# Kernel tuning notes

Measured on AMD Instinct MI355X. Metric: run time of the kernel, lower is better.

The kernel has to match this reference:

```python
import jax, jax.numpy as jnp
import numpy as np

DIM = 1024
N_HEADS = 16
HEAD_DIM = DIM // N_HEADS
COND_DIM = 1024
MLP_RATIO = 4
B = 8
L = 1024  # per-sequence length (equal lengths -> T = B*L packed tokens)
T = B * L
EPS = 1e-5


def setup_inputs() -> dict:
    key = jax.random.key(0)
    ks = jax.random.split(key, 16)
    s = 0.02
    # rotary tables: [max_pos, head_dim//2]
    inv_freq = 1.0 / (10000.0 ** (jnp.arange(0, HEAD_DIM, 2, dtype=jnp.float32) / HEAD_DIM))
    t = jnp.arange(L, dtype=jnp.float32)
    freqs = t[:, None] * inv_freq[None, :]  # [L, HEAD_DIM//2]
    return {
        "x": jax.random.normal(ks[0], (T, DIM), jnp.float32),
        "lengths": jnp.full((B,), L, dtype=jnp.int64),
        "offsets": jnp.arange(B, dtype=jnp.int64) * L,
        "cos": jnp.cos(freqs),
        "sin": jnp.sin(freqs),
        "positions": jnp.tile(jnp.arange(L, dtype=jnp.int64), B),
        "c": jax.random.normal(ks[1], (B, COND_DIM), jnp.float32),
        "ln1_w": jnp.ones((DIM,), jnp.float32),
        "Wq": jax.random.normal(ks[2], (DIM, DIM), jnp.float32) * s,
        "Wk": jax.random.normal(ks[3], (DIM, DIM), jnp.float32) * s,
        "Wv": jax.random.normal(ks[4], (DIM, DIM), jnp.float32) * s,
        "Wo": jax.random.normal(ks[5], (DIM, DIM), jnp.float32) * s,
        "ln2_w": jnp.ones((DIM,), jnp.float32),
        "W1": jax.random.normal(ks[6], (DIM, MLP_RATIO * DIM), jnp.float32) * s,
        "b1": jnp.zeros((MLP_RATIO * DIM,), jnp.float32),
        "W2": jax.random.normal(ks[7], (MLP_RATIO * DIM, DIM), jnp.float32) * s,
        "b2": jnp.zeros((DIM,), jnp.float32),
        "ada_w": jax.random.normal(ks[8], (COND_DIM, 6 * DIM), jnp.float32) * s,
        "ada_b": jnp.zeros((6 * DIM,), jnp.float32),
    }


def _layer_norm(x, w):
    # LayerNorm with weight only (no bias), as in the torch module
    mu = jnp.mean(x, axis=-1, keepdims=True)
    var = jnp.mean(jnp.square(x - mu), axis=-1, keepdims=True)
    return (x - mu) * jax.lax.rsqrt(var + EPS) * w


def _rope(q, k, cos, sin, positions):
    # q, k: [T, H, D]; cos/sin: [max_pos, D//2]; half-split RoPE
    c = cos[positions][:, None, :]  # [T, 1, D//2]
    s = sin[positions][:, None, :]
    def rot(x):
        x1, x2 = jnp.split(x, 2, axis=-1)
        return jnp.concatenate([x1 * c - x2 * s, x2 * c + x1 * s], axis=-1)
    return rot(q), rot(k)


def reference(x, lengths, offsets, cos, sin, positions, c,
              ln1_w, Wq, Wk, Wv, Wo, ln2_w, W1, b1, W2, b2, ada_w, ada_b):
    # adaLN modulation: [B, 6*DIM] -> six [B, DIM]
    ada = c @ ada_w + ada_b
    sh_msa, sc_msa, g_msa, sh_mlp, sc_mlp, g_mlp = jnp.split(ada, 6, axis=-1)
    # per-token gather via seq_ids (equal lengths -> repeat each row L times)
    seq_ids = jnp.repeat(jnp.arange(B), L)  # = repeat_interleave(arange(B), lengths)
    sh_msa_t, sc_msa_t, g_msa_t = sh_msa[seq_ids], sc_msa[seq_ids], g_msa[seq_ids]
    sh_mlp_t, sc_mlp_t, g_mlp_t = sh_mlp[seq_ids], sc_mlp[seq_ids], g_mlp[seq_ids]

    x_skip = x
    h = _layer_norm(x, ln1_w) * (1.0 + sc_msa_t) + sh_msa_t
    q = (h @ Wq).reshape(T, N_HEADS, HEAD_DIM)
    k = (h @ Wk).reshape(T, N_HEADS, HEAD_DIM)
    v = (h @ Wv).reshape(T, N_HEADS, HEAD_DIM)
    q, k = _rope(q, k, cos, sin, positions)

    # intra-sequence-only attention: with equal lengths the block-diagonal
    # score_mod mask is exactly per-sequence attention -> reshape to [B, L, H, D]
    qb = q.reshape(B, L, N_HEADS, HEAD_DIM)
    kb = k.reshape(B, L, N_HEADS, HEAD_DIM)
    vb = v.reshape(B, L, N_HEADS, HEAD_DIM)
    scores = jnp.einsum('blhd,bmhd->bhlm', qb, kb) / jnp.sqrt(jnp.float32(HEAD_DIM))
    probs = jax.nn.softmax(scores, axis=-1)
    attn = jnp.einsum('bhlm,bmhd->blhd', probs, vb).reshape(T, DIM)

    x = x_skip + g_msa_t * (attn @ Wo)  # dropout p is identity in eval mode

    h2 = _layer_norm(x, ln2_w) * (1.0 + sc_mlp_t) + sh_mlp_t
    mlp = jax.nn.gelu(h2 @ W1 + b1, approximate=True) @ W2 + b2
    return x + g_mlp_t * mlp
```

## Files before the change

kernel.cpp:

```cpp
#include <hip/hip_runtime.h>

typedef unsigned short u16;
typedef __attribute__((ext_vector_type(8))) short short8;
typedef __attribute__((ext_vector_type(4))) float f32x4;
typedef __attribute__((ext_vector_type(4))) unsigned uint4v;

__device__ __forceinline__ float bf2f(u16 u){
  unsigned v = ((unsigned)u) << 16;
  return __builtin_bit_cast(float, v);
}
__device__ __forceinline__ u16 f2bf(float f){
  unsigned u = __builtin_bit_cast(unsigned, f);
  u += 0x7fff + ((u >> 16) & 1);
  return (u16)(u >> 16);
}
__device__ __forceinline__ unsigned packbf(float lo, float hi){
  return ((unsigned)f2bf(hi) << 16) | (unsigned)f2bf(lo);
}
__device__ __forceinline__ void async16(const void* g, void* l){
  __builtin_amdgcn_global_load_lds((const __attribute__((address_space(1))) void*)g,
                                   (__attribute__((address_space(3))) void*)l, 16, 0, 0);
}
#define VMW(n) asm volatile("s_waitcnt vmcnt(" #n ")" ::: "memory")

__global__ __launch_bounds__(256) void ada_partial(
    const float* __restrict__ c, const float* __restrict__ aw,
    float* __restrict__ part){
  int n  = blockIdx.x*256 + threadIdx.x;
  int b  = blockIdx.y;
  int kc = blockIdx.z;
  const float* cr  = c + b*1024 + kc*128;
  const float* awp = aw + (size_t)(kc*128)*6144 + n;
  float acc = 0.f;
#pragma unroll 8
  for (int k = 0; k < 128; ++k)
    acc += cr[k] * awp[(size_t)k*6144];
  part[(size_t)(kc*8 + b)*6144 + n] = acc;
}

__global__ __launch_bounds__(256) void ada_reduce(
    const float* __restrict__ part, const float* __restrict__ ab,
    float* __restrict__ ada){
  int idx = blockIdx.x*256 + threadIdx.x;
  int n = idx % 6144;
  float acc = ab[n];
#pragma unroll
  for (int kc = 0; kc < 8; ++kc)
    acc += part[(size_t)kc*49152 + idx];
  ada[idx] = acc;
}

__global__ __launch_bounds__(256) void transpose_cast(
    const float* __restrict__ src, u16* __restrict__ dst, int K, int N){
  __shared__ float t[64][65];
  int n0 = blockIdx.x*64, k0 = blockIdx.y*64;
  int tid = threadIdx.x;
  int cc = tid & 63, r4 = tid >> 6;
#pragma unroll 4
  for (int it = 0; it < 16; ++it){
    int r = it*4 + r4;
    t[r][cc] = src[(size_t)(k0 + r)*N + n0 + cc];
  }
  __syncthreads();
#pragma unroll 4
  for (int it = 0; it < 16; ++it){
    int r = it*4 + r4;
    dst[(size_t)(n0 + r)*K + k0 + cc] = f2bf(t[cc][r]);
  }
}

__global__ __launch_bounds__(256) void ln_mod(
    const float* __restrict__ x, u16* __restrict__ out,
    const float* __restrict__ w, const float* __restrict__ ada,
    int shift_off, int scale_off){
  int t = blockIdx.x, tid = threadIdx.x;
  const float* xr = x + (size_t)t*1024;
  float v[4]; float s = 0.f, ss = 0.f;
#pragma unroll
  for (int i = 0; i < 4; ++i){ v[i] = xr[tid + i*256]; s += v[i]; ss += v[i]*v[i]; }
  for (int d = 1; d < 64; d <<= 1){ s += __shfl_xor(s, d); ss += __shfl_xor(ss, d); }
  __shared__ float red[8];
  int wv = tid >> 6;
  if ((tid & 63) == 0){ red[wv] = s; red[4+wv] = ss; }
  __syncthreads();
  s = red[0]+red[1]+red[2]+red[3];
  ss = red[4]+red[5]+red[6]+red[7];
  float mu = s * (1.f/1024.f);
  float var = ss * (1.f/1024.f) - mu*mu;
  float rs = rsqrtf(var + 1e-5f);
  int b = t >> 10;
  const float* sh = ada + b*6144 + shift_off;
  const float* sc = ada + b*6144 + scale_off;
#pragma unroll
  for (int i = 0; i < 4; ++i){
    int cidx = tid + i*256;
    float hh = (v[i]-mu)*rs*w[cidx]*(1.f + sc[cidx]) + sh[cidx];
    out[(size_t)t*1024 + cidx] = f2bf(hh);
  }
}

template<int EPI>
__global__ __launch_bounds__(512, 2) void gemm_bt(
    const u16* __restrict__ A, const u16* __restrict__ Bt,
    void* __restrict__ Cout, int M, int N, int K, int m_off,
    const float* __restrict__ e0, const float* __restrict__ e1,
    const float* __restrict__ e2){
  __shared__ u16 lds[65536];
  const int tid = threadIdx.x;
  const int wv = tid >> 6, lane = tid & 63;
  const int quad = lane >> 4, ln = lane & 15;
  const int wr = wv >> 2, wc = wv & 3;
  const int n0 = blockIdx.x*256, m0 = blockIdx.y*256;
  const int nt = K >> 5;

  const u16* Ap = A  + (size_t)(m0 + wv*16 + (lane>>2))*K + (lane&3)*8;
  const u16* Bp = Bt + (size_t)(n0 + wv*16 + (lane>>2))*K + (lane&3)*8;
  const size_t hstep = (size_t)128*K;
  u16* lw = lds + wv*512;

  f32x4 acc[8][4] = {};

#pragma unroll
  for (int tau = 0; tau < 3; ++tau){
    u16* d = lw + tau*16384;
    async16(Ap + (size_t)tau*32,         d);
    async16(Ap + hstep + (size_t)tau*32, d + 4096);
    async16(Bp + (size_t)tau*32,         d + 8192);
    async16(Bp + hstep + (size_t)tau*32, d + 12288);
  }
  VMW(8);
  __builtin_amdgcn_s_barrier();

  const u16* Ar = lds + (wr*128 + ln)*32 + quad*8;
  const u16* Br = lds + 8192 + (wc*64 + ln)*32 + quad*8;

  for (int t = 0; t < nt; ++t){
    const int bo = (t & 3)*16384;
    short8 bfr[4], af[4];
#pragma unroll
    for (int j = 0; j < 4; ++j) bfr[j] = *(const short8*)(Br + bo + j*512);
#pragma unroll
    for (int i = 0; i < 4; ++i) af[i]  = *(const short8*)(Ar + bo + i*512);
    if (t + 3 < nt){
      u16* d = lw + ((t+3)&3)*16384;
      async16(Ap + (size_t)(t+3)*32,         d);
      async16(Ap + hstep + (size_t)(t+3)*32, d + 4096);
    }
    __builtin_amdgcn_s_barrier();
    __builtin_amdgcn_s_setprio(1);
#pragma unroll
    for (int i = 0; i < 4; ++i)
#pragma unroll
      for (int j = 0; j < 4; ++j)
        acc[i][j] = __builtin_amdgcn_mfma_f32_16x16x32_bf16(af[i], bfr[j], acc[i][j], 0, 0, 0);
    __builtin_amdgcn_s_setprio(0);
    __builtin_amdgcn_s_barrier();
#pragma unroll
    for (int i = 0; i < 4; ++i) af[i] = *(const short8*)(Ar + bo + 2048 + i*512);
    if (t + 3 < nt){
      u16* d = lw + ((t+3)&3)*16384;
      async16(Bp + (size_t)(t+3)*32,         d + 8192);
      async16(Bp + hstep + (size_t)(t+3)*32, d + 12288);
    }
    __builtin_amdgcn_s_barrier();
    __builtin_amdgcn_s_setprio(1);
#pragma unroll
    for (int i = 0; i < 4; ++i)
#pragma unroll
      for (int j = 0; j < 4; ++j)
        acc[4+i][j] = __builtin_amdgcn_mfma_f32_16x16x32_bf16(af[i], bfr[j], acc[4+i][j], 0, 0, 0);
    __builtin_amdgcn_s_setprio(0);
    if (t + 4 <= nt)      VMW(8);
    else if (t + 3 == nt) VMW(4);
    else if (t + 2 == nt) VMW(0);
    __builtin_amdgcn_s_barrier();
  }

  const int mB = m0 + wr*128 + quad*4;
  const int nB = n0 + wc*64 + ln;
#pragma unroll
  for (int i = 0; i < 8; ++i){
#pragma unroll
    for (int r = 0; r < 4; ++r){
      const int m = mB + i*16 + r;
#pragma unroll
      for (int j = 0; j < 4; ++j){
        const int n = nB + j*16;
        float v = acc[i][j][r];
        if (EPI == 0){
          ((u16*)Cout)[(size_t)m*N + n] = f2bf(v);
        } else if (EPI == 1){
          const int b = (m + m_off) >> 10;
          float g = e1[b*6144 + 2048 + n];
          ((float*)Cout)[(size_t)m*N + n] = e0[(size_t)m*N + n] + g*v;
        } else if (EPI == 2){
          float xx = v + e0[n];
          float u = xx*(1.5957691216f + 0.07135481626f*xx*xx);
          ((u16*)Cout)[(size_t)m*N + n] = f2bf(xx / (1.f + __expf(-u)));
        } else {
          const int b = (m + m_off) >> 10;
          float g = e1[b*6144 + 5120 + n];
          ((float*)Cout)[(size_t)m*N + n] = e2[(size_t)m*N + n] + g*(v + e0[n]);
        }
      }
    }
  }
}

__global__ __launch_bounds__(256) void rope_pack(
    const u16* __restrict__ qkv, const float* __restrict__ cosT,
    const float* __restrict__ sinT, u16* __restrict__ qp,
    u16* __restrict__ kp, u16* __restrict__ vt){
  int blk = blockIdx.x;
  int lt = blk & 15, h = (blk >> 4) & 15, b = blk >> 8;
  int l0 = lt*64;
  int bh = b*16 + h;
  __shared__ u16 vl[64][68];
  int tid = threadIdx.x;
  size_t tile_base = (size_t)bh*65536 + (size_t)lt*4096;
#pragma unroll 4
  for (int it = 0; it < 16; ++it){
    int idx = it*256 + tid;
    int r = idx >> 6, d = idx & 63;
    int t = b*1024 + l0 + r;
    int pos = l0 + r;
    const u16* row = qkv + (size_t)t*3072 + h*64;
    float qv = bf2f(row[d]), kv = bf2f(row[1024+d]);
    float qo, ko;
    if (d < 32){
      float cs = cosT[pos*32 + d], sn = sinT[pos*32 + d];
      qo = qv*cs - bf2f(row[d+32])*sn;
      ko = kv*cs - bf2f(row[1024+d+32])*sn;
    } else {
      int dd = d - 32;
      float cs = cosT[pos*32 + dd], sn = sinT[pos*32 + dd];
      qo = qv*cs + bf2f(row[d-32])*sn;
      ko = kv*cs + bf2f(row[1024+d-32])*sn;
    }
    qp[((size_t)bh*1024 + l0 + r)*64 + d] = f2bf(qo*0.125f);
    kp[tile_base + (d>>5)*2048 + r*32 + (d&31)] = f2bf(ko);
    vl[d][r] = row[2048 + d];
  }
  __syncthreads();
#pragma unroll 4
  for (int it = 0; it < 16; ++it){
    int idx = it*256 + tid;
    int d = idx >> 6, cc = idx & 63;
    vt[tile_base + (cc>>5)*2048 + d*32 + (cc&31)] = vl[d][cc];
  }
}

__global__ __launch_bounds__(256) void attn_kernel(
    const u16* __restrict__ qp, const u16* __restrict__ kp,
    const u16* __restrict__ vtp, u16* __restrict__ ao){
  __shared__ u16 Kb[4096];
  __shared__ u16 Vb[4096];
  int tid = threadIdx.x, w = tid >> 6, lane = tid & 63;
  int quad = lane >> 4, ln = lane & 15;
  int bh = blockIdx.x >> 4, qb = blockIdx.x & 15;
  int h = bh & 15, b = bh >> 4;
  const u16* Q  = qp  + ((size_t)bh*1024 + qb*64 + w*16)*64;
  const u16* Kg = kp  + (size_t)bh*65536;
  const u16* Vg = vtp + (size_t)bh*65536;
  short8 qf0 = *(const short8*)(Q + ln*64 + quad*8);
  short8 qf1 = *(const short8*)(Q + ln*64 + 32 + quad*8);
  f32x4 o[4] = {};
  float m = -3e38f, l = 0.f;
  for (int kt = 0; kt < 16; ++kt){
    const u16* ktg = Kg + kt*4096 + lane*8;
    const u16* vtg = Vg + kt*4096 + lane*8;
    async16(ktg + (w*2+0)*512, Kb + (w*2+0)*512);
    async16(ktg + (w*2+1)*512, Kb + (w*2+1)*512);
    async16(vtg + (w*2+0)*512, Vb + (w*2+0)*512);
    async16(vtg + (w*2+1)*512, Vb + (w*2+1)*512);
    __syncthreads();
    f32x4 zz = {0.f, 0.f, 0.f, 0.f};
    f32x4 st[4];
#pragma unroll
    for (int c = 0; c < 4; ++c){
      short8 k0 = *(const short8*)(Kb +        (c*16 + ln)*32 + quad*8);
      short8 k1 = *(const short8*)(Kb + 2048 + (c*16 + ln)*32 + quad*8);
      st[c] = __builtin_amdgcn_mfma_f32_16x16x32_bf16(k0, qf0, zz, 0,0,0);
      st[c] = __builtin_amdgcn_mfma_f32_16x16x32_bf16(k1, qf1, st[c], 0,0,0);
    }
    short8 va[4][2];
#pragma unroll
    for (int dc = 0; dc < 4; ++dc)
#pragma unroll
      for (int kh = 0; kh < 2; ++kh)
        va[dc][kh] = *(const short8*)(Vb + kh*2048 + (dc*16 + ln)*32 + quad*8);
    float mx = st[0][0];
#pragma unroll
    for (int c = 0; c < 4; ++c)
#pragma unroll
      for (int r = 0; r < 4; ++r) mx = fmaxf(mx, st[c][r]);
    mx = fmaxf(mx, __shfl_xor(mx, 16));
    mx = fmaxf(mx, __shfl_xor(mx, 32));
    float mn = fmaxf(m, mx);
    float alpha = __expf(m - mn);
    m = mn;
    float p[4][4];
#pragma unroll
    for (int c = 0; c < 4; ++c)
#pragma unroll
      for (int r = 0; r < 4; ++r) p[c][r] = __expf(st[c][r] - mn);
    float sum = ((p[0][0]+p[0][1]) + (p[0][2]+p[0][3])) + ((p[1][0]+p[1][1]) + (p[1][2]+p[1][3]))
              + ((p[2][0]+p[2][1]) + (p[2][2]+p[2][3])) + ((p[3][0]+p[3][1]) + (p[3][2]+p[3][3]));
    sum += __shfl_xor(sum, 16);
    sum += __shfl_xor(sum, 32);
    l = l*alpha + sum;
#pragma unroll
    for (int dc = 0; dc < 4; ++dc)
#pragma unroll
      for (int r = 0; r < 4; ++r) o[dc][r] *= alpha;
    unsigned pc[4][2];
#pragma unroll
    for (int c = 0; c < 4; ++c){
      pc[c][0] = packbf(p[c][0], p[c][1]);
      pc[c][1] = packbf(p[c][2], p[c][3]);
    }
    const int sA = ((quad & 1)*2)*16 + ln;
    const int sB = sA + 16;
    const bool hi = quad >= 2;
#pragma unroll
    for (int kh = 0; kh < 2; ++kh){
      unsigned a0 = (unsigned)__shfl((int)pc[2*kh][0],   sA);
      unsigned b0 = (unsigned)__shfl((int)pc[2*kh+1][0], sA);
      unsigned a1 = (unsigned)__shfl((int)pc[2*kh][1],   sA);
      unsigned b1 = (unsigned)__shfl((int)pc[2*kh+1][1], sA);
      unsigned a2 = (unsigned)__shfl((int)pc[2*kh][0],   sB);
      unsigned b2 = (unsigned)__shfl((int)pc[2*kh+1][0], sB);
      unsigned a3 = (unsigned)__shfl((int)pc[2*kh][1],   sB);
      unsigned b3 = (unsigned)__shfl((int)pc[2*kh+1][1], sB);
      uint4v u = { hi ? b0 : a0, hi ? b1 : a1, hi ? b2 : a2, hi ? b3 : a3 };
      short8 pfrag = __builtin_bit_cast(short8, u);
#pragma unroll
      for (int dc = 0; dc < 4; ++dc)
        o[dc] = __builtin_amdgcn_mfma_f32_16x16x32_bf16(va[dc][kh], pfrag, o[dc], 0,0,0);
    }
    __syncthreads();
  }
  float rl = 1.f / l;
  size_t orow = ((size_t)b*1024 + qb*64 + w*16 + ln)*1024 + h*64;
#pragma unroll
  for (int dc = 0; dc < 4; ++dc)
#pragma unroll
    for (int r = 0; r < 4; ++r)
      ao[orow + dc*16 + quad*4 + r] = f2bf(o[dc][r] * rl);
}

extern "C" void kernel_launch(void* const* d_in, const int* in_sizes, int n_in,
                              void* d_out, int out_size, void* d_ws, size_t ws_size,
                              hipStream_t stream){
  const float* x    = (const float*)d_in[0];
  const float* cosT = (const float*)d_in[3];
  const float* sinT = (const float*)d_in[4];
  const float* c    = (const float*)d_in[6];
  const float* ln1w = (const float*)d_in[7];
  const float* Wq   = (const float*)d_in[8];
  const float* Wk   = (const float*)d_in[9];
  const float* Wv   = (const float*)d_in[10];
  const float* Wo   = (const float*)d_in[11];
  const float* ln2w = (const float*)d_in[12];
  const float* W1   = (const float*)d_in[13];
  const float* b1   = (const float*)d_in[14];
  const float* W2   = (const float*)d_in[15];
  const float* b2   = (const float*)d_in[16];
  const float* adaW = (const float*)d_in[17];
  const float* adaB = (const float*)d_in[18];

  char* ws = (char*)d_ws;
  float* ada  = (float*)(ws);
  u16* wqkvt  = (u16*)  (ws + 262144);
  u16* wot    = (u16*)  (ws + 6553600);
  u16* w1t    = (u16*)  (ws + 8650752);
  u16* w2t    = (u16*)  (ws + 17039360);
  u16* h      = (u16*)  (ws + 25427968);
  u16* qp     = (u16*)  (ws + 25427968);
  u16* h2     = (u16*)  (ws + 25427968);
  u16* qkv    = (u16*)  (ws + 42205184);
  u16* attnb  = (u16*)  (ws + 42205184);
  float* xmid = (float*)(ws + 58982400);
  float* adaP = (float*)(ws + 92536832);
  u16* kp     = (u16*)  (ws + 92536832);
  u16* vt     = (u16*)  (ws + 109314048);
  u16* hid    = (u16*)  (ws + 92536832);
  u16* hidF   = (u16*)  (ws + 126091264);
  float* out  = (float*)d_out;
  const bool bigws = ws_size >= (size_t)193200128;

  ada_partial<<<dim3(24,8,8), 256, 0, stream>>>(c, adaW, adaP);
  ada_reduce<<<192, 256, 0, stream>>>(adaP, adaB, ada);
  transpose_cast<<<dim3(16,16), 256, 0, stream>>>(Wq, wqkvt,             1024, 1024);
  transpose_cast<<<dim3(16,16), 256, 0, stream>>>(Wk, wqkvt + 1024*1024, 1024, 1024);
  transpose_cast<<<dim3(16,16), 256, 0, stream>>>(Wv, wqkvt + 2048*1024, 1024, 1024);
  transpose_cast<<<dim3(16,16), 256, 0, stream>>>(Wo, wot,               1024, 1024);
  transpose_cast<<<dim3(64,16), 256, 0, stream>>>(W1, w1t,               1024, 4096);
  transpose_cast<<<dim3(16,64), 256, 0, stream>>>(W2, w2t,               4096, 1024);
  ln_mod<<<8192, 256, 0, stream>>>(x, h, ln1w, ada, 0, 1024);
  gemm_bt<0><<<dim3(12,32), 512, 0, stream>>>(h, wqkvt, qkv, 8192, 3072, 1024, 0,
                                              nullptr, nullptr, nullptr);
  rope_pack<<<2048, 256, 0, stream>>>(qkv, cosT, sinT, qp, kp, vt);
  attn_kernel<<<2048, 256, 0, stream>>>(qp, kp, vt, attnb);
  gemm_bt<1><<<dim3(4,32), 512, 0, stream>>>(attnb, wot, xmid, 8192, 1024, 1024, 0,
                                             x, ada, nullptr);
  ln_mod<<<8192, 256, 0, stream>>>(xmid, h2, ln2w, ada, 3072, 4096);
  if (bigws){
    gemm_bt<2><<<dim3(16,32), 512, 0, stream>>>(h2, w1t, hidF, 8192, 4096, 1024, 0,
                                                b1, nullptr, nullptr);
    gemm_bt<3><<<dim3(4,32), 512, 0, stream>>>(hidF, w2t, out, 8192, 1024, 4096, 0,
                                               b2, ada, xmid);
  } else {
    for (int cch = 0; cch < 2; ++cch){
      const size_t mo = (size_t)cch*4096;
      gemm_bt<2><<<dim3(16,16), 512, 0, stream>>>(h2 + mo*1024, w1t, hid,
                                                  4096, 4096, 1024, (int)mo,
                                                  b1, nullptr, nullptr);
      gemm_bt<3><<<dim3(4,16), 512, 0, stream>>>(hid, w2t, out + mo*1024,
                                                 4096, 1024, 4096, (int)mo,
                                                 b2, ada, xmid + mo*1024);
    }
  }
}
```

Measured before the change: 664.2 us.

## Add 128x128-tile GEMM variant and XOR-swizzle LDS layout to avoid bank conflicts

```diff
diff --git a/kernel.cpp b/kernel.cpp
--- a/kernel.cpp
+++ b/kernel.cpp
@@ -100,6 +100,27 @@
 }
 
 template<int EPI>
+__device__ __forceinline__ void gemm_epi(
+    void* Cout, int m, int n, int N, int m_off, float v,
+    const float* e0, const float* e1, const float* e2){
+  if (EPI == 0){
+    ((u16*)Cout)[(size_t)m*N + n] = f2bf(v);
+  } else if (EPI == 1){
+    const int b = (m + m_off) >> 10;
+    float g = e1[b*6144 + 2048 + n];
+    ((float*)Cout)[(size_t)m*N + n] = e0[(size_t)m*N + n] + g*v;
+  } else if (EPI == 2){
+    float xx = v + e0[n];
+    float u = xx*(1.5957691216f + 0.07135481626f*xx*xx);
+    ((u16*)Cout)[(size_t)m*N + n] = f2bf(xx / (1.f + __expf(-u)));
+  } else {
+    const int b = (m + m_off) >> 10;
+    float g = e1[b*6144 + 5120 + n];
+    ((float*)Cout)[(size_t)m*N + n] = e2[(size_t)m*N + n] + g*(v + e0[n]);
+  }
+}
+
+template<int EPI>
 __global__ __launch_bounds__(512, 2) void gemm_bt(
     const u16* __restrict__ A, const u16* __restrict__ Bt,
     void* __restrict__ Cout, int M, int N, int K, int m_off,
@@ -113,8 +134,9 @@
   const int n0 = blockIdx.x*256, m0 = blockIdx.y*256;
   const int nt = K >> 5;
 
-  const u16* Ap = A  + (size_t)(m0 + wv*16 + (lane>>2))*K + (lane&3)*8;
-  const u16* Bp = Bt + (size_t)(n0 + wv*16 + (lane>>2))*K + (lane&3)*8;
+  const int swslot = (lane & 3) ^ ((lane >> 3) & 3);
+  const u16* Ap = A  + (size_t)(m0 + wv*16 + (lane>>2))*K + swslot*8;
+  const u16* Bp = Bt + (size_t)(n0 + wv*16 + (lane>>2))*K + swslot*8;
   const size_t hstep = (size_t)128*K;
   u16* lw = lds + wv*512;
 
@@ -131,8 +153,9 @@
   VMW(8);
   __builtin_amdgcn_s_barrier();
 
-  const u16* Ar = lds + (wr*128 + ln)*32 + quad*8;
-  const u16* Br = lds + 8192 + (wc*64 + ln)*32 + quad*8;
+  const int rsw = (quad ^ ((ln >> 1) & 3))*8;
+  const u16* Ar = lds + (wr*128 + ln)*32 + rsw;
+  const u16* Br = lds + 8192 + (wc*64 + ln)*32 + rsw;
 
   for (int t = 0; t < nt; ++t){
     const int bo = (t & 3)*16384;
@@ -179,32 +202,102 @@
   const int mB = m0 + wr*128 + quad*4;
   const int nB = n0 + wc*64 + ln;
 #pragma unroll
-  for (int i = 0; i < 8; ++i){
-#pragma unroll
-    for (int r = 0; r < 4; ++r){
-      const int m = mB + i*16 + r;
-#pragma unroll
-      for (int j = 0; j < 4; ++j){
-        const int n = nB + j*16;
-        float v = acc[i][j][r];
-        if (EPI == 0){
-          ((u16*)Cout)[(size_t)m*N + n] = f2bf(v);
-        } else if (EPI == 1){
-          const int b = (m + m_off) >> 10;
-          float g = e1[b*6144 + 2048 + n];
-          ((float*)Cout)[(size_t)m*N + n] = e0[(size_t)m*N + n] + g*v;
-        } else if (EPI == 2){
-          float xx = v + e0[n];
-          float u = xx*(1.5957691216f + 0.07135481626f*xx*xx);
-          ((u16*)Cout)[(size_t)m*N + n] = f2bf(xx / (1.f + __expf(-u)));
-        } else {
-          const int b = (m + m_off) >> 10;
-          float g = e1[b*6144 + 5120 + n];
-          ((float*)Cout)[(size_t)m*N + n] = e2[(size_t)m*N + n] + g*(v + e0[n]);
-        }
-      }
-    }
-  }
+  for (int i = 0; i < 8; ++i)
+#pragma unroll
+    for (int r = 0; r < 4; ++r)
+#pragma unroll
+      for (int j = 0; j < 4; ++j)
+        gemm_epi<EPI>(Cout, mB + i*16 + r, nB + j*16, N, m_off, acc[i][j][r], e0, e1, e2);
+}
+
+template<int EPI>
+__global__ __launch_bounds__(256, 2) void gemm_bt128(
+    const u16* __restrict__ A, const u16* __restrict__ Bt,
+    void* __restrict__ Cout, int M, int N, int K, int m_off,
+    const float* __restrict__ e0, const float* __restrict__ e1,
+    const float* __restrict__ e2){
+  __shared__ u16 lds[32768];
+  const int tid = threadIdx.x;
+  const int wv = tid >> 6, lane = tid & 63;
+  const int quad = lane >> 4, ln = lane & 15;
+  const int wr = wv >> 1, wc = wv & 1;
+  const int n0 = blockIdx.x*128, m0 = blockIdx.y*128;
+  const int nt = K >> 5;
+
+  const int swslot = (lane & 3) ^ ((lane >> 3) & 3);
+  const u16* Ap = A  + (size_t)(m0 + wv*16 + (lane>>2))*K + swslot*8;
+  const u16* Bp = Bt + (size_t)(n0 + wv*16 + (lane>>2))*K + swslot*8;
+  const size_t hstep = (size_t)64*K;
+  u16* lw = lds + wv*512;
+
+  f32x4 acc[4][4] = {};
+
+#pragma unroll
+  for (int tau = 0; tau < 3; ++tau){
+    u16* d = lw + tau*8192;
+    async16(Ap + (size_t)tau*32,         d);
+    async16(Ap + hstep + (size_t)tau*32, d + 2048);
+    async16(Bp + (size_t)tau*32,         d + 4096);
+    async16(Bp + hstep + (size_t)tau*32, d + 6144);
+  }
+  VMW(8);
+  __builtin_amdgcn_s_barrier();
+
+  const int rsw = (quad ^ ((ln >> 1) & 3))*8;
+  const u16* Ar = lds + (wr*64 + ln)*32 + rsw;
+  const u16* Br = lds + 4096 + (wc*64 + ln)*32 + rsw;
+
+  for (int t = 0; t < nt; ++t){
+    const int bo = (t & 3)*8192;
+    short8 bfr[4], af[2];
+#pragma unroll
+    for (int j = 0; j < 4; ++j) bfr[j] = *(const short8*)(Br + bo + j*512);
+#pragma unroll
+    for (int i = 0; i < 2; ++i) af[i]  = *(const short8*)(Ar + bo + i*512);
+    if (t + 3 < nt){
+      u16* d = lw + ((t+3)&3)*8192;
+      async16(Ap + (size_t)(t+3)*32,         d);
+      async16(Ap + hstep + (size_t)(t+3)*32, d + 2048);
+    }
+    __builtin_amdgcn_s_barrier();
+    __builtin_amdgcn_s_setprio(1);
+#pragma unroll
+    for (int i = 0; i < 2; ++i)
+#pragma unroll
+      for (int j = 0; j < 4; ++j)
+        acc[i][j] = __builtin_amdgcn_mfma_f32_16x16x32_bf16(af[i], bfr[j], acc[i][j], 0, 0, 0);
+    __builtin_amdgcn_s_setprio(0);
+    __builtin_amdgcn_s_barrier();
+#pragma unroll
+    for (int i = 0; i < 2; ++i) af[i] = *(const short8*)(Ar + bo + 1024 + i*512);
+    if (t + 3 < nt){
+      u16* d = lw + ((t+3)&3)*8192;
+      async16(Bp + (size_t)(t+3)*32,         d + 4096);
+      async16(Bp + hstep + (size_t)(t+3)*32, d + 6144);
+    }
+    __builtin_amdgcn_s_barrier();
+    __builtin_amdgcn_s_setprio(1);
+#pragma unroll
+    for (int i = 0; i < 2; ++i)
+#pragma unroll
+      for (int j = 0; j < 4; ++j)
+        acc[2+i][j] = __builtin_amdgcn_mfma_f32_16x16x32_bf16(af[i], bfr[j], acc[2+i][j], 0, 0, 0);
+    __builtin_amdgcn_s_setprio(0);
+    if (t + 4 <= nt)      VMW(8);
+    else if (t + 3 == nt) VMW(4);
+    else if (t + 2 == nt) VMW(0);
+    __builtin_amdgcn_s_barrier();
+  }
+
+  const int mB = m0 + wr*64 + quad*4;
+  const int nB = n0 + wc*64 + ln;
+#pragma unroll
+  for (int i = 0; i < 4; ++i)
+#pragma unroll
+    for (int r = 0; r < 4; ++r)
+#pragma unroll
+      for (int j = 0; j < 4; ++j)
+        gemm_epi<EPI>(Cout, mB + i*16 + r, nB + j*16, N, m_off, acc[i][j][r], e0, e1, e2);
 }
 
 __global__ __launch_bounds__(256) void rope_pack(
@@ -398,27 +491,27 @@
   transpose_cast<<<dim3(64,16), 256, 0, stream>>>(W1, w1t,               1024, 4096);
   transpose_cast<<<dim3(16,64), 256, 0, stream>>>(W2, w2t,               4096, 1024);
   ln_mod<<<8192, 256, 0, stream>>>(x, h, ln1w, ada, 0, 1024);
-  gemm_bt<0><<<dim3(12,32), 512, 0, stream>>>(h, wqkvt, qkv, 8192, 3072, 1024, 0,
-                                              nullptr, nullptr, nullptr);
+  gemm_bt128<0><<<dim3(24,64), 256, 0, stream>>>(h, wqkvt, qkv, 8192, 3072, 1024, 0,
+                                                 nullptr, nullptr, nullptr);
   rope_pack<<<2048, 256, 0, stream>>>(qkv, cosT, sinT, qp, kp, vt);
   attn_kernel<<<2048, 256, 0, stream>>>(qp, kp, vt, attnb);
-  gemm_bt<1><<<dim3(4,32), 512, 0, stream>>>(attnb, wot, xmid, 8192, 1024, 1024, 0,
-                                             x, ada, nullptr);
+  gemm_bt128<1><<<dim3(8,64), 256, 0, stream>>>(attnb, wot, xmid, 8192, 1024, 1024, 0,
+                                                x, ada, nullptr);
   ln_mod<<<8192, 256, 0, stream>>>(xmid, h2, ln2w, ada, 3072, 4096);
   if (bigws){
     gemm_bt<2><<<dim3(16,32), 512, 0, stream>>>(h2, w1t, hidF, 8192, 4096, 1024, 0,
                                                 b1, nullptr, nullptr);
-    gemm_bt<3><<<dim3(4,32), 512, 0, stream>>>(hidF, w2t, out, 8192, 1024, 4096, 0,
-                                               b2, ada, xmid);
+    gemm_bt128<3><<<dim3(8,64), 256, 0, stream>>>(hidF, w2t, out, 8192, 1024, 4096, 0,
+                                                  b2, ada, xmid);
   } else {
     for (int cch = 0; cch < 2; ++cch){
       const size_t mo = (size_t)cch*4096;
       gemm_bt<2><<<dim3(16,16), 512, 0, stream>>>(h2 + mo*1024, w1t, hid,
                                                   4096, 4096, 1024, (int)mo,
                                                   b1, nullptr, nullptr);
-      gemm_bt<3><<<dim3(4,16), 512, 0, stream>>>(hid, w2t, out + mo*1024,
-                                                 4096, 1024, 4096, (int)mo,
-                                                 b2, ada, xmid + mo*1024);
-    }
-  }
-}
+      gemm_bt128<3><<<dim3(8,32), 256, 0, stream>>>(hid, w2t, out + mo*1024,
+                                                    4096, 1024, 4096, (int)mo,
+                                                    b2, ada, xmid + mo*1024);
+    }
+  }
+}
```

New measurement: 601.6 us. 1.1x faster.
